# Kernel tuning notes

Hardware: AMD Instinct MI355X
Metric: run time of the kernel (lower is better)

Reference implementation:

```python
import jax, jax.numpy as jnp
import numpy as np

SEQ_LEN, IN_CH, OUT_CH, H, BATCH = 2048, 16, 1, 80, 512


def _lstm(x, W_ih, W_hh, b_ih, b_hh):
    """Single-layer batch-first LSTM (PyTorch gate order i,f,g,o).
    x: [B, T, D]. Returns (outputs [B, T, H], last hidden [B, H])."""
    B = x.shape[0]
    h0 = jnp.zeros((B, H), x.dtype)
    c0 = jnp.zeros((B, H), x.dtype)
    # Precompute input projections for all timesteps in one GEMM: [T, B, 4H]
    xproj = jnp.einsum('btd,gd->tbg', x, W_ih) + (b_ih + b_hh)

    def step(carry, xp_t):
        h, c = carry
        gates = xp_t + h @ W_hh.T  # [B, 4H]
        i, f, g, o = jnp.split(gates, 4, axis=-1)
        i = jax.nn.sigmoid(i)
        f = jax.nn.sigmoid(f)
        g = jnp.tanh(g)
        o = jax.nn.sigmoid(o)
        c = f * c + i * g
        h = o * jnp.tanh(c)
        return (h, c), h

    (h_last, _), hs = jax.lax.scan(step, (h0, c0), xproj)
    return jnp.swapaxes(hs, 0, 1), h_last


def setup_inputs() -> dict:
    key = jax.random.key(0)
    ks = jax.random.split(key, 12)
    s1 = 1.0 / np.sqrt(H)
    d = {
        'x': jax.random.normal(ks[0], (BATCH, SEQ_LEN, IN_CH), jnp.float32),
        'W_ih1': jax.random.uniform(ks[1], (4 * H, IN_CH), jnp.float32, -s1, s1),
        'W_hh1': jax.random.uniform(ks[2], (4 * H, H), jnp.float32, -s1, s1),
        'b_ih1': jax.random.uniform(ks[3], (4 * H,), jnp.float32, -s1, s1),
        'b_hh1': jax.random.uniform(ks[4], (4 * H,), jnp.float32, -s1, s1),
        'W_ih2': jax.random.uniform(ks[5], (4 * H, H), jnp.float32, -s1, s1),
        'W_hh2': jax.random.uniform(ks[6], (4 * H, H), jnp.float32, -s1, s1),
        'b_ih2': jax.random.uniform(ks[7], (4 * H,), jnp.float32, -s1, s1),
        'b_hh2': jax.random.uniform(ks[8], (4 * H,), jnp.float32, -s1, s1),
        'W_d': jax.random.uniform(ks[9], (OUT_CH, H), jnp.float32, -s1, s1),
        'b_d': jax.random.uniform(ks[10], (OUT_CH,), jnp.float32, -s1, s1),
    }
    return d


def reference(x, W_ih1, W_hh1, b_ih1, b_hh1, W_ih2, W_hh2, b_ih2, b_hh2, W_d, b_d):
    B = x.shape[0]
    x = x.reshape((B, SEQ_LEN, IN_CH))
    y1, _ = _lstm(x, W_ih1, W_hh1, b_ih1, b_hh1)          # [B, T, H]
    _, h_last = _lstm(y1, W_ih2, W_hh2, b_ih2, b_hh2)     # [B, H]
    return h_last @ W_d.T + b_d                           # [B, OUT_CH]
```

## Files before the change

kernel.cpp:

```cpp
#include <hip/hip_runtime.h>

#define T_SEQ 2048
#define DIN   16
#define HH    80
#define NTHR  512
#define NBLK  256
#define BT    2
#define ROWE  192

#define L2E   1.44269504088896340736f

typedef _Float16 f16x8 __attribute__((ext_vector_type(8)));
typedef float    f32x4 __attribute__((ext_vector_type(4)));

__device__ __forceinline__ float rcp_fast(float x){ return __builtin_amdgcn_rcpf(x); }
__device__ __forceinline__ float ex2(float x){
#if __has_builtin(__builtin_amdgcn_exp2f)
    return __builtin_amdgcn_exp2f(x);
#else
    return exp2f(x);
#endif
}

#define MF(av, bv, cv) __builtin_amdgcn_mfma_f32_16x16x32_f16(av, bv, cv, 0, 0, 0)
#define L1SLOT(acc, s) { acc = MF(A[s][0], B0, Q[s]); acc = MF(A[s][1], B1, acc); \
                         acc = MF(A[s][2], B2, acc); }
#define L2SLOT(acc, s) { acc = MF(A[s][0], B0, Q[s]); acc = MF(A[s][1], B1, acc); \
                         acc = MF(A[s][2], B2, acc); acc = MF(A[s][3], B3, acc); \
                         acc = MF(A[s][4], B4, acc); }

#define SPIN2(pa, ta, pb, tb) { int _s = 0; \
    while ((__hip_atomic_load((pa), __ATOMIC_RELAXED, __HIP_MEMORY_SCOPE_WORKGROUP) < (ta)) || \
           (__hip_atomic_load((pb), __ATOMIC_RELAXED, __HIP_MEMORY_SCOPE_WORKGROUP) < (tb))) { \
        if (++_s > (1<<14)) break; } \
    __builtin_amdgcn_fence(__ATOMIC_ACQUIRE, "workgroup"); }

#define SIGNAL(p) if (lane == 0) \
    __hip_atomic_fetch_add((p), 1, __ATOMIC_RELEASE, __HIP_MEMORY_SCOPE_WORKGROUP)

__global__
__attribute__((amdgpu_flat_work_group_size(NTHR, NTHR)))
__attribute__((amdgpu_waves_per_eu(2, 2)))
void lstm2_flag(
    const float* __restrict__ x,
    const float* __restrict__ W_ih1, const float* __restrict__ W_hh1,
    const float* __restrict__ b_ih1, const float* __restrict__ b_hh1,
    const float* __restrict__ W_ih2, const float* __restrict__ W_hh2,
    const float* __restrict__ b_ih2, const float* __restrict__ b_hh2,
    const float* __restrict__ W_d,   const float* __restrict__ b_d,
    float* __restrict__ out)
{
    __shared__ __align__(16) _Float16 HB[2][BT][ROWE];
    __shared__ int W1c;
    __shared__ int W2c;
    __shared__ int RD2c;

    const int t    = threadIdx.x;
    const int lane = t & 63;
    const int wv   = t >> 6;
    const bool isL1w = (wv < 4);
    const int m16  = lane & 15;
    const int kgrp = lane >> 4;
    const int b0   = blockIdx.x * BT;

    const int uloc = isL1w ? 20*wv : 20*(wv-4);

    f16x8 A[5][5];
    f32x4 Q[5];
    {
        const int g  = m16 & 3;
        const int ut = m16 >> 2;
        const float sc = (g == 2) ? (2.f*L2E) : L2E;
        #pragma unroll
        for (int s = 0; s < 5; ++s) {
            const int grow = g*HH + (uloc + 4*s + ut);
            #pragma unroll
            for (int c = 0; c < 5; ++c) {
                if (isL1w && c >= 3) continue;
                f16x8 a;
                #pragma unroll
                for (int j = 0; j < 8; ++j) {
                    const int kk = 32*c + 8*kgrp + j;
                    const float v = isL1w
                        ? ((kk < DIN) ? W_ih1[(size_t)grow*DIN + kk]
                                      : W_hh1[(size_t)grow*HH + (kk - DIN)])
                        : ((kk < HH)  ? W_ih2[(size_t)grow*HH + kk]
                                      : W_hh2[(size_t)grow*HH + (kk - HH)]);
                    a[j] = (_Float16)(v * sc);
                }
                A[s][c] = a;
            }
            const int u = uloc + 4*s + kgrp;
            const float* bI = isL1w ? b_ih1 : b_ih2;
            const float* bH = isL1w ? b_hh1 : b_hh2;
            f32x4 bb;
            bb[0] = (bI[       u] + bH[       u]) * L2E;
            bb[1] = (bI[  HH + u] + bH[  HH + u]) * L2E;
            bb[2] = (bI[2*HH + u] + bH[2*HH + u]) * (2.f*L2E);
            bb[3] = (bI[3*HH + u] + bH[3*HH + u]) * L2E;
            Q[s] = bb;
        }
    }

    const int  te      = m16 >> 1;
    const bool act_ep  = (m16 < 10);
    const int  unit_ep = uloc + 4*(act_ep ? te : 0) + kgrp;
    const int  seg     = isL1w ? DIN : (DIN + HH);
    const int  batch_ep = lane & 1;

    for (int i = t; i < 2*BT*ROWE; i += NTHR) ((_Float16*)HB)[i] = (_Float16)0.f;
    if (t == 0) { W1c = 0; W2c = 0; RD2c = 0; }

    const int xbn = (lane >> 4) & 1;
    const int xch = lane & 15;
    const float* xptr = x + ((size_t)(b0 + xbn) * T_SEQ) * DIN + xch;
    float xa = 0.f, xbv = 0.f, xcv = 0.f;
    if (wv == 0 && lane < 32) {
        HB[0][xbn][xch] = (_Float16)xptr[0];
        xa  = xptr[1*DIN];
        xbv = xptr[2*DIN];
        xcv = xptr[3*DIN];
    }
    __syncthreads();

    float cst = 0.f;

    #pragma unroll 1
    for (int k = 0; k <= T_SEQ; ++k) {
        const int pb = k & 1, nb = pb ^ 1;

        if (isL1w) {
            SPIN2(&W1c, 4*k, &RD2c, 4*k);

            if (wv == 0 && lane < 32) {
                HB[nb][xbn][xch] = (_Float16)xa;
                xa = xbv; xbv = xcv;
                const int tn = (k + 4 < T_SEQ) ? (k + 4) : (T_SEQ - 1);
                xcv = xptr[(size_t)tn * DIN];
            }

            if (k < T_SEQ) {
                const _Float16* rb = &HB[pb][lane & 1][0];
                const f16x8 B0 = *(const f16x8*)(rb +       8*kgrp);
                const f16x8 B1 = *(const f16x8*)(rb +  32 + 8*kgrp);
                const f16x8 B2 = *(const f16x8*)(rb +  64 + 8*kgrp);
                f32x4 acc0, acc1, acc2, acc3, acc4;
                L1SLOT(acc0, 0) L1SLOT(acc1, 1) L1SLOT(acc2, 2)
                L1SLOT(acc3, 3) L1SLOT(acc4, 4)

                float M0 = acc0[0], M1 = acc0[1], M2 = acc0[2], M3 = acc0[3];
                if (te == 1) { M0 = acc1[0]; M1 = acc1[1]; M2 = acc1[2]; M3 = acc1[3]; }
                if (te == 2) { M0 = acc2[0]; M1 = acc2[1]; M2 = acc2[2]; M3 = acc2[3]; }
                if (te == 3) { M0 = acc3[0]; M1 = acc3[1]; M2 = acc3[2]; M3 = acc3[3]; }
                if (te == 4) { M0 = acc4[0]; M1 = acc4[1]; M2 = acc4[2]; M3 = acc4[3]; }

                const float iv = rcp_fast(1.f + ex2(-M0));
                const float fv = rcp_fast(1.f + ex2(-M1));
                const float gv = 1.f - 2.f*rcp_fast(1.f + ex2(M2));
                const float ov = rcp_fast(1.f + ex2(-M3));
                cst = fv*cst + iv*gv;
                const float tc = 1.f - 2.f*rcp_fast(1.f + ex2(cst * (2.f*L2E)));
                if (act_ep)
                    HB[nb][batch_ep][seg + unit_ep] = (_Float16)(ov * tc);
            }
            asm volatile("s_waitcnt lgkmcnt(0)" ::: "memory");
            SIGNAL(&W1c);
        } else {
            SPIN2(&W1c, 4*k, &W2c, 4*k);

            f16x8 B0{}, B1{}, B2{}, B3{}, B4{};
            if (k >= 1) {
                const _Float16* rb = &HB[pb][lane & 1][0];
                B0 = *(const f16x8*)(rb +  16 + 8*kgrp);
                B1 = *(const f16x8*)(rb +  48 + 8*kgrp);
                B2 = *(const f16x8*)(rb +  80 + 8*kgrp);
                B3 = *(const f16x8*)(rb + 112 + 8*kgrp);
                B4 = *(const f16x8*)(rb + 144 + 8*kgrp);
            }
            asm volatile("s_waitcnt lgkmcnt(0)" ::: "memory");
            SIGNAL(&RD2c);

            if (k >= 1) {
                f32x4 acc0, acc1, acc2, acc3, acc4;
                L2SLOT(acc0, 0) L2SLOT(acc1, 1) L2SLOT(acc2, 2)
                L2SLOT(acc3, 3) L2SLOT(acc4, 4)

                float M0 = acc0[0], M1 = acc0[1], M2 = acc0[2], M3 = acc0[3];
                if (te == 1) { M0 = acc1[0]; M1 = acc1[1]; M2 = acc1[2]; M3 = acc1[3]; }
                if (te == 2) { M0 = acc2[0]; M1 = acc2[1]; M2 = acc2[2]; M3 = acc2[3]; }
                if (te == 3) { M0 = acc3[0]; M1 = acc3[1]; M2 = acc3[2]; M3 = acc3[3]; }
                if (te == 4) { M0 = acc4[0]; M1 = acc4[1]; M2 = acc4[2]; M3 = acc4[3]; }

                const float iv = rcp_fast(1.f + ex2(-M0));
                const float fv = rcp_fast(1.f + ex2(-M1));
                const float gv = 1.f - 2.f*rcp_fast(1.f + ex2(M2));
                const float ov = rcp_fast(1.f + ex2(-M3));
                cst = fv*cst + iv*gv;
                const float tc = 1.f - 2.f*rcp_fast(1.f + ex2(cst * (2.f*L2E)));
                if (act_ep)
                    HB[nb][batch_ep][seg + unit_ep] = (_Float16)(ov * tc);
            }
            asm volatile("s_waitcnt lgkmcnt(0)" ::: "memory");
            SIGNAL(&W2c);
        }
    }

    if (wv == 0) {
        SPIN2(&W2c, 4*(T_SEQ+1), &W1c, 0);
        float a0 = 0.f, a1 = 0.f;
        for (int u = lane; u < HH; u += 64) {
            const float wd = W_d[u];
            a0 += wd * (float)HB[1][0][DIN + HH + u];
            a1 += wd * (float)HB[1][1][DIN + HH + u];
        }
        #pragma unroll
        for (int off = 32; off > 0; off >>= 1) {
            a0 += __shfl_down(a0, off);
            a1 += __shfl_down(a1, off);
        }
        if (lane == 0) { out[b0] = a0 + b_d[0]; out[b0 + 1] = a1 + b_d[0]; }
    }
}

extern "C" void kernel_launch(void* const* d_in, const int* in_sizes, int n_in,
                              void* d_out, int out_size, void* d_ws, size_t ws_size,
                              hipStream_t stream) {
    const float* x     = (const float*)d_in[0];
    const float* W_ih1 = (const float*)d_in[1];
    const float* W_hh1 = (const float*)d_in[2];
    const float* b_ih1 = (const float*)d_in[3];
    const float* b_hh1 = (const float*)d_in[4];
    const float* W_ih2 = (const float*)d_in[5];
    const float* W_hh2 = (const float*)d_in[6];
    const float* b_ih2 = (const float*)d_in[7];
    const float* b_hh2 = (const float*)d_in[8];
    const float* W_d   = (const float*)d_in[9];
    const float* b_d   = (const float*)d_in[10];

    lstm2_flag<<<NBLK, NTHR, 0, stream>>>(x, W_ih1, W_hh1, b_ih1, b_hh1,
                                          W_ih2, W_hh2, b_ih2, b_hh2,
                                          W_d, b_d, (float*)d_out);
}
```

Before: 1.584 ms.

## Replace spin-flag wave sync with block barriers and pin weight registers

Removes the shared-memory atomic flag handshake between layer-1 and layer-2 waves and uses a single __syncthreads per timestep instead. Weight fragments and biases are stored as float4 arrays and pinned in VGPRs with empty asm constraints to prevent reloading or spilling. This drops atomic polling overhead and the bounded spin loop. It also gives up the early read-signal overlap that let layer-1 run ahead while layer-2 computed.

After: 1.447 ms. 1.09x faster.

```diff
diff --git a/kernel.cpp b/kernel.cpp
--- a/kernel.cpp
+++ b/kernel.cpp
@@ -23,25 +23,27 @@
 }
 
 #define MF(av, bv, cv) __builtin_amdgcn_mfma_f32_16x16x32_f16(av, bv, cv, 0, 0, 0)
-#define L1SLOT(acc, s) { acc = MF(A[s][0], B0, Q[s]); acc = MF(A[s][1], B1, acc); \
-                         acc = MF(A[s][2], B2, acc); }
-#define L2SLOT(acc, s) { acc = MF(A[s][0], B0, Q[s]); acc = MF(A[s][1], B1, acc); \
-                         acc = MF(A[s][2], B2, acc); acc = MF(A[s][3], B3, acc); \
-                         acc = MF(A[s][4], B4, acc); }
-
-#define SPIN2(pa, ta, pb, tb) { int _s = 0; \
-    while ((__hip_atomic_load((pa), __ATOMIC_RELAXED, __HIP_MEMORY_SCOPE_WORKGROUP) < (ta)) || \
-           (__hip_atomic_load((pb), __ATOMIC_RELAXED, __HIP_MEMORY_SCOPE_WORKGROUP) < (tb))) { \
-        if (++_s > (1<<14)) break; } \
-    __builtin_amdgcn_fence(__ATOMIC_ACQUIRE, "workgroup"); }
-
-#define SIGNAL(p) if (lane == 0) \
-    __hip_atomic_fetch_add((p), 1, __ATOMIC_RELEASE, __HIP_MEMORY_SCOPE_WORKGROUP)
+#define FA(i) __builtin_bit_cast(f16x8, AV[i])
+#define FQ(s) __builtin_bit_cast(f32x4, QV[s])
+
+#define L1SLOT(acc, s) { acc = MF(FA(s*5+0), B0, FQ(s)); acc = MF(FA(s*5+1), B1, acc); \
+                         acc = MF(FA(s*5+2), B2, acc); }
+#define L2SLOT(acc, s) { acc = MF(FA(s*5+0), B0, FQ(s)); acc = MF(FA(s*5+1), B1, acc); \
+                         acc = MF(FA(s*5+2), B2, acc); acc = MF(FA(s*5+3), B3, acc); \
+                         acc = MF(FA(s*5+4), B4, acc); }
+
+#define PIN4(v) asm volatile("" : "+v"(v.x), "+v"(v.y), "+v"(v.z), "+v"(v.w))
+#define PIN_ALL { PIN4(AV[0]);  PIN4(AV[1]);  PIN4(AV[2]);  PIN4(AV[3]);  PIN4(AV[4]);  \
+                  PIN4(AV[5]);  PIN4(AV[6]);  PIN4(AV[7]);  PIN4(AV[8]);  PIN4(AV[9]);  \
+                  PIN4(AV[10]); PIN4(AV[11]); PIN4(AV[12]); PIN4(AV[13]); PIN4(AV[14]); \
+                  PIN4(AV[15]); PIN4(AV[16]); PIN4(AV[17]); PIN4(AV[18]); PIN4(AV[19]); \
+                  PIN4(AV[20]); PIN4(AV[21]); PIN4(AV[22]); PIN4(AV[23]); PIN4(AV[24]); \
+                  PIN4(QV[0]);  PIN4(QV[1]);  PIN4(QV[2]);  PIN4(QV[3]);  PIN4(QV[4]); }
 
 __global__
 __attribute__((amdgpu_flat_work_group_size(NTHR, NTHR)))
 __attribute__((amdgpu_waves_per_eu(2, 2)))
-void lstm2_flag(
+void lstm2_mfma(
     const float* __restrict__ x,
     const float* __restrict__ W_ih1, const float* __restrict__ W_hh1,
     const float* __restrict__ b_ih1, const float* __restrict__ b_hh1,
@@ -51,9 +53,6 @@
     float* __restrict__ out)
 {
     __shared__ __align__(16) _Float16 HB[2][BT][ROWE];
-    __shared__ int W1c;
-    __shared__ int W2c;
-    __shared__ int RD2c;
 
     const int t    = threadIdx.x;
     const int lane = t & 63;
@@ -65,8 +64,8 @@
 
     const int uloc = isL1w ? 20*wv : 20*(wv-4);
 
-    f16x8 A[5][5];
-    f32x4 Q[5];
+    float4 AV[25];
+    float4 QV[5];
     {
         const int g  = m16 & 3;
         const int ut = m16 >> 2;
@@ -76,7 +75,7 @@
             const int grow = g*HH + (uloc + 4*s + ut);
             #pragma unroll
             for (int c = 0; c < 5; ++c) {
-                if (isL1w && c >= 3) continue;
+                if (isL1w && c >= 3) { AV[s*5+c] = make_float4(0.f,0.f,0.f,0.f); continue; }
                 f16x8 a;
                 #pragma unroll
                 for (int j = 0; j < 8; ++j) {
@@ -88,17 +87,15 @@
                                       : W_hh2[(size_t)grow*HH + (kk - HH)]);
                     a[j] = (_Float16)(v * sc);
                 }
-                A[s][c] = a;
+                AV[s*5+c] = __builtin_bit_cast(float4, a);
             }
             const int u = uloc + 4*s + kgrp;
             const float* bI = isL1w ? b_ih1 : b_ih2;
             const float* bH = isL1w ? b_hh1 : b_hh2;
-            f32x4 bb;
-            bb[0] = (bI[       u] + bH[       u]) * L2E;
-            bb[1] = (bI[  HH + u] + bH[  HH + u]) * L2E;
-            bb[2] = (bI[2*HH + u] + bH[2*HH + u]) * (2.f*L2E);
-            bb[3] = (bI[3*HH + u] + bH[3*HH + u]) * L2E;
-            Q[s] = bb;
+            QV[s] = make_float4((bI[       u] + bH[       u]) * L2E,
+                                (bI[  HH + u] + bH[  HH + u]) * L2E,
+                                (bI[2*HH + u] + bH[2*HH + u]) * (2.f*L2E),
+                                (bI[3*HH + u] + bH[3*HH + u]) * L2E);
         }
     }
 
@@ -109,7 +106,7 @@
     const int  batch_ep = lane & 1;
 
     for (int i = t; i < 2*BT*ROWE; i += NTHR) ((_Float16*)HB)[i] = (_Float16)0.f;
-    if (t == 0) { W1c = 0; W2c = 0; RD2c = 0; }
+    __syncthreads();
 
     const int xbn = (lane >> 4) & 1;
     const int xch = lane & 15;
@@ -128,85 +125,54 @@
     #pragma unroll 1
     for (int k = 0; k <= T_SEQ; ++k) {
         const int pb = k & 1, nb = pb ^ 1;
-
-        if (isL1w) {
-            SPIN2(&W1c, 4*k, &RD2c, 4*k);
-
-            if (wv == 0 && lane < 32) {
-                HB[nb][xbn][xch] = (_Float16)xa;
-                xa = xbv; xbv = xcv;
-                const int tn = (k + 4 < T_SEQ) ? (k + 4) : (T_SEQ - 1);
-                xcv = xptr[(size_t)tn * DIN];
-            }
-
-            if (k < T_SEQ) {
-                const _Float16* rb = &HB[pb][lane & 1][0];
+        PIN_ALL;
+
+        if (wv == 0 && lane < 32) {
+            HB[nb][xbn][xch] = (_Float16)xa;
+            xa = xbv; xbv = xcv;
+            const int tn = (k + 4 < T_SEQ) ? (k + 4) : (T_SEQ - 1);
+            xcv = xptr[(size_t)tn * DIN];
+        }
+
+        const bool act = isL1w ? (k < T_SEQ) : (k >= 1);
+        if (act) {
+            const _Float16* rb = &HB[pb][lane & 1][0];
+            f32x4 acc0, acc1, acc2, acc3, acc4;
+            if (isL1w) {
                 const f16x8 B0 = *(const f16x8*)(rb +       8*kgrp);
                 const f16x8 B1 = *(const f16x8*)(rb +  32 + 8*kgrp);
                 const f16x8 B2 = *(const f16x8*)(rb +  64 + 8*kgrp);
-                f32x4 acc0, acc1, acc2, acc3, acc4;
                 L1SLOT(acc0, 0) L1SLOT(acc1, 1) L1SLOT(acc2, 2)
                 L1SLOT(acc3, 3) L1SLOT(acc4, 4)
-
-                float M0 = acc0[0], M1 = acc0[1], M2 = acc0[2], M3 = acc0[3];
-                if (te == 1) { M0 = acc1[0]; M1 = acc1[1]; M2 = acc1[2]; M3 = acc1[3]; }
-                if (te == 2) { M0 = acc2[0]; M1 = acc2[1]; M2 = acc2[2]; M3 = acc2[3]; }
-                if (te == 3) { M0 = acc3[0]; M1 = acc3[1]; M2 = acc3[2]; M3 = acc3[3]; }
-                if (te == 4) { M0 = acc4[0]; M1 = acc4[1]; M2 = acc4[2]; M3 = acc4[3]; }
-
-                const float iv = rcp_fast(1.f + ex2(-M0));
-                const float fv = rcp_fast(1.f + ex2(-M1));
-                const float gv = 1.f - 2.f*rcp_fast(1.f + ex2(M2));
-                const float ov = rcp_fast(1.f + ex2(-M3));
-                cst = fv*cst + iv*gv;
-                const float tc = 1.f - 2.f*rcp_fast(1.f + ex2(cst * (2.f*L2E)));
-                if (act_ep)
-                    HB[nb][batch_ep][seg + unit_ep] = (_Float16)(ov * tc);
-            }
-            asm volatile("s_waitcnt lgkmcnt(0)" ::: "memory");
-            SIGNAL(&W1c);
-        } else {
-            SPIN2(&W1c, 4*k, &W2c, 4*k);
-
-            f16x8 B0{}, B1{}, B2{}, B3{}, B4{};
-            if (k >= 1) {
-                const _Float16* rb = &HB[pb][lane & 1][0];
-                B0 = *(const f16x8*)(rb +  16 + 8*kgrp);
-                B1 = *(const f16x8*)(rb +  48 + 8*kgrp);
-                B2 = *(const f16x8*)(rb +  80 + 8*kgrp);
-                B3 = *(const f16x8*)(rb + 112 + 8*kgrp);
-                B4 = *(const f16x8*)(rb + 144 + 8*kgrp);
-            }
-            asm volatile("s_waitcnt lgkmcnt(0)" ::: "memory");
-            SIGNAL(&RD2c);
-
-            if (k >= 1) {
-                f32x4 acc0, acc1, acc2, acc3, acc4;
+            } else {
+                const f16x8 B0 = *(const f16x8*)(rb +  16 + 8*kgrp);
+                const f16x8 B1 = *(const f16x8*)(rb +  48 + 8*kgrp);
+                const f16x8 B2 = *(const f16x8*)(rb +  80 + 8*kgrp);
+                const f16x8 B3 = *(const f16x8*)(rb + 112 + 8*kgrp);
+                const f16x8 B4 = *(const f16x8*)(rb + 144 + 8*kgrp);
                 L2SLOT(acc0, 0) L2SLOT(acc1, 1) L2SLOT(acc2, 2)
                 L2SLOT(acc3, 3) L2SLOT(acc4, 4)
-
-                float M0 = acc0[0], M1 = acc0[1], M2 = acc0[2], M3 = acc0[3];
-                if (te == 1) { M0 = acc1[0]; M1 = acc1[1]; M2 = acc1[2]; M3 = acc1[3]; }
-                if (te == 2) { M0 = acc2[0]; M1 = acc2[1]; M2 = acc2[2]; M3 = acc2[3]; }
-                if (te == 3) { M0 = acc3[0]; M1 = acc3[1]; M2 = acc3[2]; M3 = acc3[3]; }
-                if (te == 4) { M0 = acc4[0]; M1 = acc4[1]; M2 = acc4[2]; M3 = acc4[3]; }
-
-                const float iv = rcp_fast(1.f + ex2(-M0));
-                const float fv = rcp_fast(1.f + ex2(-M1));
-                const float gv = 1.f - 2.f*rcp_fast(1.f + ex2(M2));
-                const float ov = rcp_fast(1.f + ex2(-M3));
-                cst = fv*cst + iv*gv;
-                const float tc = 1.f - 2.f*rcp_fast(1.f + ex2(cst * (2.f*L2E)));
-                if (act_ep)
-                    HB[nb][batch_ep][seg + unit_ep] = (_Float16)(ov * tc);
             }
-            asm volatile("s_waitcnt lgkmcnt(0)" ::: "memory");
-            SIGNAL(&W2c);
-        }
+
+            float M0 = acc0[0], M1 = acc0[1], M2 = acc0[2], M3 = acc0[3];
+            if (te == 1) { M0 = acc1[0]; M1 = acc1[1]; M2 = acc1[2]; M3 = acc1[3]; }
+            if (te == 2) { M0 = acc2[0]; M1 = acc2[1]; M2 = acc2[2]; M3 = acc2[3]; }
+            if (te == 3) { M0 = acc3[0]; M1 = acc3[1]; M2 = acc3[2]; M3 = acc3[3]; }
+            if (te == 4) { M0 = acc4[0]; M1 = acc4[1]; M2 = acc4[2]; M3 = acc4[3]; }
+
+            const float iv = rcp_fast(1.f + ex2(-M0));
+            const float fv = rcp_fast(1.f + ex2(-M1));
+            const float gv = 1.f - 2.f*rcp_fast(1.f + ex2(M2));
+            const float ov = rcp_fast(1.f + ex2(-M3));
+            cst = fv*cst + iv*gv;
+            const float tc = 1.f - 2.f*rcp_fast(1.f + ex2(cst * (2.f*L2E)));
+            if (act_ep)
+                HB[nb][batch_ep][seg + unit_ep] = (_Float16)(ov * tc);
+        }
+        __syncthreads();
     }
 
     if (wv == 0) {
-        SPIN2(&W2c, 4*(T_SEQ+1), &W1c, 0);
         float a0 = 0.f, a1 = 0.f;
         for (int u = lane; u < HH; u += 64) {
             const float wd = W_d[u];
@@ -237,7 +203,7 @@
     const float* W_d   = (const float*)d_in[9];
     const float* b_d   = (const float*)d_in[10];
 
-    lstm2_flag<<<NBLK, NTHR, 0, stream>>>(x, W_ih1, W_hh1, b_ih1, b_hh1,
+    lstm2_mfma<<<NBLK, NTHR, 0, stream>>>(x, W_ih1, W_hh1, b_ih1, b_hh1,
                                           W_ih2, W_hh2, b_ih2, b_hh2,
                                           W_d, b_d, (float*)d_out);
 }
```
